# Kernel tuning notes

Hardware: AMD Instinct MI355X
Metric: run time of the kernel (lower is better)

The kernel has to match this reference:

```python
import jax, jax.numpy as jnp
import numpy as np

B, F, H, W = 1, 4, 20, 44
P = H * W            # 880 tokens per frame (20*44, from max_attention_size = 15*880)
S = F * P            # 3520 packed tokens
DIM, NH, FFN, OUT = 1536, 12, 6144, 64   # OUT = prod(patch_size)*out_dim = 4*16
HD = DIM // NH       # 128
C = HD // 2          # 64 rotary complex pairs
EPS = 1e-6


def _rope_angles():
    # Wan 3D RoPE: split C pairs as (C-2*(C//3), C//3, C//3) over (frame, h, w)
    cf, ch, cw = C - 2 * (C // 3), C // 3, C // 3
    def tab(n, cp):
        inv = 1.0 / (10000.0 ** (np.arange(cp) / cp))
        return np.outer(np.arange(n), inv)
    af = np.broadcast_to(tab(F, cf)[:, None, None, :], (F, H, W, cf))
    ah = np.broadcast_to(tab(H, ch)[None, :, None, :], (F, H, W, ch))
    aw = np.broadcast_to(tab(W, cw)[None, None, :, :], (F, H, W, cw))
    return np.concatenate([af, ah, aw], -1).reshape(S, C).astype(np.float32)


def setup_inputs() -> dict:
    key = jax.random.key(0)
    ks = jax.random.split(key, 24)
    g = lambda i, shape, s=0.02: jax.random.normal(ks[i], shape, dtype=jnp.float32) * s
    inp = {
        'x': jax.random.normal(ks[0], (B, S, DIM), dtype=jnp.float32),
        'e': g(1, (B, F, 6, DIM), 1.0),
        'e_head': g(2, (B, F, 2, DIM), 1.0),
        'rope_angles': jnp.asarray(_rope_angles()),
        'mod_block': g(3, (1, 6, DIM), 1.0 / float(np.sqrt(DIM))),
        'mod_head': g(4, (1, 2, DIM), 1.0 / float(np.sqrt(DIM))),
        'Wq': g(5, (DIM, DIM)), 'bq': jnp.zeros((DIM,), jnp.float32),
        'Wk': g(6, (DIM, DIM)), 'bk': jnp.zeros((DIM,), jnp.float32),
        'Wv': g(7, (DIM, DIM)), 'bv': jnp.zeros((DIM,), jnp.float32),
        'Wo': g(8, (DIM, DIM)), 'bo': jnp.zeros((DIM,), jnp.float32),
        'wq_norm': jnp.ones((DIM,), jnp.float32),
        'wk_norm': jnp.ones((DIM,), jnp.float32),
        'W1': g(9, (DIM, FFN)), 'b1': jnp.zeros((FFN,), jnp.float32),
        'W2': g(10, (FFN, DIM)), 'b2': jnp.zeros((DIM,), jnp.float32),
        'Wh': g(11, (DIM, OUT)), 'bh': jnp.zeros((OUT,), jnp.float32),
    }
    return inp


def _ln(x):
    # WanLayerNorm without elementwise affine
    m = jnp.mean(x, axis=-1, keepdims=True)
    v = jnp.var(x, axis=-1, keepdims=True)
    return (x - m) * jax.lax.rsqrt(v + EPS)


def _rms(x, w):
    return x * jax.lax.rsqrt(jnp.mean(x * x, axis=-1, keepdims=True) + EPS) * w


def _rope(t, ang):
    # t: [B,S,NH,HD]; adjacent pairs form complex numbers (view_as_complex style)
    tr = t.reshape(B, S, NH, C, 2)
    cos = jnp.cos(ang)[None, :, None, :]
    sin = jnp.sin(ang)[None, :, None, :]
    t0, t1 = tr[..., 0], tr[..., 1]
    return jnp.stack([t0 * cos - t1 * sin, t0 * sin + t1 * cos], -1).reshape(B, S, NH, HD)


def reference(x, e, e_head, rope_angles, mod_block, mod_head,
              Wq, bq, Wk, bk, Wv, bv, Wo, bo, wq_norm, wk_norm,
              W1, b1, W2, b2, Wh, bh):
    # ---- AdaLN modulation split (6-way) ----
    em = mod_block[:, None] + e                      # [B,F,6,DIM]
    e0, e1, e2, e3, e4, e5 = [em[:, :, i][:, :, None, :] for i in range(6)]

    xf = x.reshape(B, F, P, DIM)
    h = (_ln(xf) * (1 + e1) + e0).reshape(B, S, DIM)

    # ---- QK-RMSNorm + RoPE self attention (block-causal, block = one frame) ----
    q = _rope(_rms(h @ Wq + bq, wq_norm).reshape(B, S, NH, HD), rope_angles)
    k = _rope(_rms(h @ Wk + bk, wk_norm).reshape(B, S, NH, HD), rope_angles)
    v = (h @ Wv + bv).reshape(B, S, NH, HD)

    blk = jnp.arange(S) // P
    mask = blk[None, :] <= blk[:, None]              # [S,S] block-causal
    scores = jnp.einsum('bqhd,bkhd->bhqk', q, k) / np.float32(np.sqrt(HD))
    scores = jnp.where(mask[None, None], scores, jnp.float32(-1e30))
    attn = jax.nn.softmax(scores, axis=-1)
    y = jnp.einsum('bhqk,bkhd->bqhd', attn, v).reshape(B, S, DIM) @ Wo + bo

    xf = xf + y.reshape(B, F, P, DIM) * e2

    # ---- FFN with AdaLN modulation ----
    hf = (_ln(xf) * (1 + e4) + e3).reshape(B, S, DIM)
    ff = jax.nn.gelu(hf @ W1 + b1) @ W2 + b2
    xf = xf + ff.reshape(B, F, P, DIM) * e5

    # ---- OutputHead: modulated norm + linear ----
    eh = mod_head[:, None] + e_head                  # [B,F,2,DIM]
    eh0 = eh[:, :, 0][:, :, None, :]
    eh1 = eh[:, :, 1][:, :, None, :]
    out = (_ln(xf) * (1 + eh1) + eh0) @ Wh + bh      # [B,F,P,OUT]
    return out
```

## Files before the change

kernel.cpp:

```cpp
#include <hip/hip_runtime.h>
#include <cstdint>
#include <cstddef>

typedef __bf16 bf16;
typedef __bf16 bf16x2 __attribute__((ext_vector_type(2)));
typedef __bf16 bf16x8 __attribute__((ext_vector_type(8)));
typedef float f32x4 __attribute__((ext_vector_type(4)));
typedef unsigned int u32x4 __attribute__((ext_vector_type(4)));

#define S_TOK 3520
#define S_PAD 3584
#define P_TOK 880
#define NFRM 4
#define DIM 1536
#define NH 12
#define HD 128
#define FFN_D 6144
#define NOUT 64
#define EPSV 1e-6f
#define QSCALE 0.12751743f

__device__ __forceinline__ f32x4 mfma16(bf16x8 a, bf16x8 b, f32x4 c) {
  return __builtin_amdgcn_mfma_f32_16x16x32_bf16(a, b, c, 0, 0, 0);
}

__device__ __forceinline__ void gload_lds16(const bf16* g, bf16* l) {
  __builtin_amdgcn_global_load_lds(
      (const __attribute__((address_space(1))) unsigned int*)g,
      (__attribute__((address_space(3))) unsigned int*)l, 16, 0, 0);
}

__device__ __forceinline__ uint32_t pk2(float lo, float hi) {
  bf16x2 t;
  t[0] = (bf16)lo;
  t[1] = (bf16)hi;
  return __builtin_bit_cast(uint32_t, t);
}

__global__ __launch_bounds__(256) void k_prep(const float* __restrict__ e,
                                              const float* __restrict__ e_head,
                                              const float* __restrict__ mod_block,
                                              const float* __restrict__ mod_head,
                                              float* __restrict__ em,
                                              float* __restrict__ ehm) {
  int i = blockIdx.x * 256 + threadIdx.x;
  if (i < NFRM * 6 * DIM) em[i] = mod_block[i % (6 * DIM)] + e[i];
  int j = i - NFRM * 6 * DIM;
  if (j >= 0 && j < NFRM * 2 * DIM) ehm[j] = mod_head[j % (2 * DIM)] + e_head[j];
}

__global__ __launch_bounds__(256) void k_zero_vpad(bf16* __restrict__ vc) {
  size_t base = ((size_t)blockIdx.x * 28 + 27) * 4096 + 2048 + (size_t)threadIdx.x * 8;
#pragma unroll
  for (int i = 0; i < 8; ++i) vc[base + i] = (bf16)0.f;
}

__global__ __launch_bounds__(256) void k_transpose(const float* __restrict__ W,
                                                   bf16* __restrict__ Wt, int K, int N) {
  __shared__ float tile[32][33];
  int n0 = blockIdx.x * 32, k0 = blockIdx.y * 32;
  int tx = threadIdx.x & 31, ty = threadIdx.x >> 5;
#pragma unroll
  for (int j = 0; j < 4; ++j) {
    int k = k0 + ty * 4 + j;
    float v = (n0 + tx < N) ? W[(size_t)k * N + n0 + tx] : 0.f;
    tile[ty * 4 + j][tx] = v;
  }
  __syncthreads();
#pragma unroll
  for (int j = 0; j < 4; ++j) {
    int n = n0 + ty * 4 + j;
    if (n < N) Wt[(size_t)n * K + k0 + tx] = (bf16)tile[tx][ty * 4 + j];
  }
}

__global__ __launch_bounds__(256) void k_adaln(const float* __restrict__ in,
                                               bf16* __restrict__ out,
                                               const float* __restrict__ e_shift,
                                               const float* __restrict__ e_scale,
                                               int fstride) {
  int tok = blockIdx.x;
  int t = threadIdx.x;
  bf16* orow = out + (size_t)tok * DIM;
  if (tok >= S_TOK) {
#pragma unroll
    for (int i = 0; i < 6; ++i) orow[t * 6 + i] = (bf16)0.f;
    return;
  }
  const float* xrow = in + (size_t)tok * DIM;
  float v[6];
  float s = 0.f, sq = 0.f;
#pragma unroll
  for (int i = 0; i < 6; ++i) {
    v[i] = xrow[t * 6 + i];
    s += v[i];
    sq += v[i] * v[i];
  }
  for (int off = 32; off; off >>= 1) {
    s += __shfl_down(s, off);
    sq += __shfl_down(sq, off);
  }
  __shared__ float red[8];
  int wv = t >> 6, lane = t & 63;
  if (lane == 0) { red[wv] = s; red[4 + wv] = sq; }
  __syncthreads();
  float ts = red[0] + red[1] + red[2] + red[3];
  float tq = red[4] + red[5] + red[6] + red[7];
  float mean = ts * (1.f / DIM);
  float var = tq * (1.f / DIM) - mean * mean;
  float rstd = rsqrtf(var + EPSV);
  int f = tok / P_TOK;
  const float* sh = e_shift + (size_t)f * fstride;
  const float* sc = e_scale + (size_t)f * fstride;
#pragma unroll
  for (int i = 0; i < 6; ++i) {
    int d = t * 6 + i;
    orow[d] = (bf16)((v[i] - mean) * rstd * (1.f + sc[d]) + sh[d]);
  }
}

__global__ __launch_bounds__(256) void k_qkv_post(const float* __restrict__ qkv,
                                                  const float* __restrict__ wqn,
                                                  const float* __restrict__ wkn,
                                                  const float* __restrict__ ang,
                                                  bf16* __restrict__ qb,
                                                  bf16* __restrict__ kb,
                                                  bf16* __restrict__ vc) {
  int s = blockIdx.x;
  int t = threadIdx.x;
  const float* row = qkv + (size_t)s * 3 * DIM;
  float qv[6], kv[6], vv[6];
  float sqq = 0.f, sqk = 0.f;
  int d0 = t * 6;
#pragma unroll
  for (int i = 0; i < 6; ++i) {
    int d = d0 + i;
    qv[i] = row[d];
    kv[i] = row[DIM + d];
    vv[i] = row[2 * DIM + d];
    sqq += qv[i] * qv[i];
    sqk += kv[i] * kv[i];
  }
  float a1 = sqq, a2 = sqk;
  for (int off = 32; off; off >>= 1) {
    a1 += __shfl_down(a1, off);
    a2 += __shfl_down(a2, off);
  }
  __shared__ float red[8];
  int wv = t >> 6, lane = t & 63;
  if (lane == 0) { red[wv] = a1; red[4 + wv] = a2; }
  __syncthreads();
  float tq = red[0] + red[1] + red[2] + red[3];
  float tk = red[4] + red[5] + red[6] + red[7];
  float rq = rsqrtf(tq * (1.f / DIM) + EPSV);
  float rk = rsqrtf(tk * (1.f / DIM) + EPSV);
#pragma unroll
  for (int p = 0; p < 3; ++p) {
    int d = d0 + p * 2;
    int h = d >> 7;
    int hd = d & 127;
    int c = hd >> 1;
    float a = ang[(size_t)s * 64 + c];
    float sa, ca;
    sincosf(a, &sa, &ca);
    float q0 = qv[p * 2] * rq * wqn[d], q1 = qv[p * 2 + 1] * rq * wqn[d + 1];
    float k0 = kv[p * 2] * rk * wkn[d], k1 = kv[p * 2 + 1] * rk * wkn[d + 1];
    size_t base = ((size_t)h * S_TOK + s) * HD + hd;
    qb[base]     = (bf16)((q0 * ca - q1 * sa) * QSCALE);
    qb[base + 1] = (bf16)((q0 * sa + q1 * ca) * QSCALE);
    kb[base]     = (bf16)(k0 * ca - k1 * sa);
    kb[base + 1] = (bf16)(k0 * sa + k1 * ca);
  }
  int f = s / P_TOK;
  int l = s - f * P_TOK;
  int lb = l >> 5, gg = (l >> 3) & 3, r = l & 7;
#pragma unroll
  for (int i = 0; i < 6; ++i) {
    int d = d0 + i;
    int h = d >> 7, hd = d & 127;
    vc[((((size_t)(h * NFRM + f)) * 28 + lb) * 512 + gg * 128 + hd) * 8 + r] = (bf16)vv[i];
  }
}

__global__ __launch_bounds__(320) void k_attn(const bf16* __restrict__ qb,
                                              const bf16* __restrict__ kb,
                                              const bf16* __restrict__ vc,
                                              float* __restrict__ parto,
                                              float* __restrict__ partml) {
  __shared__ __align__(16) bf16 Ks[512 * 8];
  __shared__ __align__(16) bf16 Vs[512 * 8];
  int h = blockIdx.x / 110;
  int p = blockIdx.x % 110;
  int f = (p < 11) ? 0 : (p < 33) ? 1 : (p < 66) ? 2 : 3;
  int cum = (f == 0) ? 0 : (f == 1) ? 11 : (f == 2) ? 33 : 66;
  int w = p - cum;
  int kc = w / 11;
  int qt = f * 11 + w % 11;
  int slot = blockIdx.x;
  int t = threadIdx.x;
  int wv = t >> 6, lane = t & 63;
  int r16 = lane & 15, g = lane >> 4;
  int q0 = qt * 80 + wv * 16;
  int kv0 = kc * P_TOK;
  const bf16* qbase = qb + ((size_t)h * S_TOK + q0 + r16) * HD + g * 8;
  bf16x8 qf[4];
#pragma unroll
  for (int kk = 0; kk < 4; ++kk) qf[kk] = *(const bf16x8*)(qbase + kk * 32);
  f32x4 acc[8] = {};
  float mrow = -1e30f, lrow = 0.f;
  int src01 = r16 + ((2 * g) & 3) * 16;
  int src23 = src01 + 16;
  bool glo = (g < 2);
  int s1 = t + 320;
  bool has1 = (s1 < 512);
  int krow0 = t >> 4, ksl0 = t & 15;
  int kss0 = (ksl0 & 8) | ((ksl0 ^ krow0) & 7);
  int krow1 = s1 >> 4, ksl1 = s1 & 15;
  int kss1 = (ksl1 & 8) | ((ksl1 ^ krow1) & 7);
  const bf16* kh = kb + (size_t)h * S_TOK * HD;
  const bf16* vchunk = vc + ((size_t)(h * NFRM + kc)) * 28 * 4096;
  const int nsteps = (P_TOK + 31) >> 5;
  for (int j = 0; j < nsteps; ++j) {
    int kvo = j * 32;
    __syncthreads();
    {
      int gr0 = kv0 + kvo + krow0;
      if (gr0 >= S_TOK) gr0 = 0;
      gload_lds16(kh + (size_t)gr0 * HD + kss0 * 8, Ks + t * 8);
      gload_lds16(vchunk + (size_t)j * 4096 + t * 8, Vs + t * 8);
      if (has1) {
        int gr1 = kv0 + kvo + krow1;
        if (gr1 >= S_TOK) gr1 = 0;
        gload_lds16(kh + (size_t)gr1 * HD + kss1 * 8, Ks + s1 * 8);
        gload_lds16(vchunk + (size_t)j * 4096 + s1 * 8, Vs + s1 * 8);
      }
    }
    __syncthreads();
    f32x4 st0 = {0.f, 0.f, 0.f, 0.f}, st1 = {0.f, 0.f, 0.f, 0.f};
#pragma unroll
    for (int kk = 0; kk < 4; ++kk) {
      int sl = g + 4 * kk;
      int ss = (sl & 8) | ((sl ^ r16) & 7);
      bf16x8 k0 = *(const bf16x8*)(Ks + (r16 * 16 + ss) * 8);
      bf16x8 k1 = *(const bf16x8*)(Ks + ((16 + r16) * 16 + ss) * 8);
      st0 = mfma16(k0, qf[kk], st0);
      st1 = mfma16(k1, qf[kk], st1);
    }
    float hm = (kvo + 16 >= P_TOK) ? -1e30f : 0.f;
    float a0[4], a1[4];
#pragma unroll
    for (int r = 0; r < 4; ++r) {
      a0[r] = st0[r];
      a1[r] = st1[r] + hm;
    }
    float tm = fmaxf(fmaxf(fmaxf(a0[0], a0[1]), fmaxf(a0[2], a0[3])),
                     fmaxf(fmaxf(a1[0], a1[1]), fmaxf(a1[2], a1[3])));
    tm = fmaxf(tm, __shfl_xor(tm, 16));
    tm = fmaxf(tm, __shfl_xor(tm, 32));
    float mn = fmaxf(mrow, tm);
    float p0[4], p1[4], ps = 0.f;
#pragma unroll
    for (int r = 0; r < 4; ++r) {
      p0[r] = exp2f(a0[r] - mn);
      p1[r] = exp2f(a1[r] - mn);
      ps += p0[r] + p1[r];
    }
    float scl = exp2f(mrow - mn);
    mrow = mn;
    lrow = lrow * scl + ps;
    uint32_t A0 = pk2(p0[0], p0[1]), A1 = pk2(p0[2], p0[3]);
    uint32_t B0 = pk2(p1[0], p1[1]), B1 = pk2(p1[2], p1[3]);
    uint32_t sA0 = __shfl(A0, src01), sA1 = __shfl(A1, src01);
    uint32_t sB0 = __shfl(B0, src01), sB1 = __shfl(B1, src01);
    uint32_t tA0 = __shfl(A0, src23), tA1 = __shfl(A1, src23);
    uint32_t tB0 = __shfl(B0, src23), tB1 = __shfl(B1, src23);
    u32x4 wds;
    wds[0] = glo ? sA0 : sB0;
    wds[1] = glo ? sA1 : sB1;
    wds[2] = glo ? tA0 : tB0;
    wds[3] = glo ? tA1 : tB1;
    bf16x8 pb = __builtin_bit_cast(bf16x8, wds);
#pragma unroll
    for (int hb = 0; hb < 8; ++hb) {
      acc[hb][0] *= scl;
      acc[hb][1] *= scl;
      acc[hb][2] *= scl;
      acc[hb][3] *= scl;
    }
    const bf16* vsl = Vs + (size_t)(g * 128 + r16) * 8;
#pragma unroll
    for (int hb = 0; hb < 8; ++hb) {
      bf16x8 vfr = *(const bf16x8*)(vsl + hb * 128);
      acc[hb] = mfma16(vfr, pb, acc[hb]);
    }
  }
  lrow += __shfl_xor(lrow, 16);
  lrow += __shfl_xor(lrow, 32);
  float* obase = parto + (((size_t)slot * 5 + wv) * 8) * 256;
#pragma unroll
  for (int hb = 0; hb < 8; ++hb) {
    *(f32x4*)(obase + (hb * 64 + lane) * 4) = acc[hb];
  }
  if (g == 0) {
    float* mlb = partml + ((size_t)slot * 5 + wv) * 32;
    mlb[r16] = mrow;
    mlb[16 + r16] = lrow;
  }
}

__global__ __launch_bounds__(256) void k_att_reduce(const float* __restrict__ parto,
                                                    const float* __restrict__ partml,
                                                    bf16* __restrict__ attb) {
  int b = blockIdx.x;
  int h = b / 44, qt = b % 44;
  int f = qt / 11, j = qt % 11;
  int cum = (f == 0) ? 0 : (f == 1) ? 11 : (f == 2) ? 33 : 66;
  int t = threadIdx.x;
  int d = t & 127, half = t >> 7;
  int hb = d >> 4, g = (d >> 2) & 3, r = d & 3;
  int q0 = qt * 80;
  for (int it = 0; it < 40; ++it) {
    int qloc = it + 40 * half;
    int wv = qloc >> 4, r16 = qloc & 15;
    float m[4], l[4];
    float mt = -1e30f;
    for (int kc = 0; kc <= f; ++kc) {
      int slot = h * 110 + cum + kc * 11 + j;
      const float* mlb = partml + ((size_t)slot * 5 + wv) * 32;
      m[kc] = mlb[r16];
      l[kc] = mlb[16 + r16];
      mt = fmaxf(mt, m[kc]);
    }
    float lt = 0.f, o = 0.f;
    for (int kc = 0; kc <= f; ++kc) {
      int slot = h * 110 + cum + kc * 11 + j;
      float wgt = exp2f(m[kc] - mt);
      lt += l[kc] * wgt;
      o += parto[(((size_t)slot * 5 + wv) * 8 + hb) * 256 + (g * 16 + r16) * 4 + r] * wgt;
    }
    attb[(size_t)(q0 + qloc) * DIM + h * HD + d] = (bf16)(o / lt);
  }
}

struct GemmP {
  const bf16* A;
  const bf16* Bt;
  int K;
  int Mtiles;
  int Ntiles;
  int Mreal;
  int mode;
  const float* bias0;
  const float* bias1;
  const float* bias2;
  const float* res;
  const float* emod;
  int e_fstride;
  float* outf;
  bf16* outb;
  int ldo;
};

__global__ __launch_bounds__(256, 2) void k_gemm(GemmP p) {
  int nwg = p.Mtiles * p.Ntiles;
  int bid = blockIdx.x;
  int l = bid;
  if ((nwg & 7) == 0) {
    int cpx = nwg >> 3;
    l = (bid & 7) * cpx + (bid >> 3);
  }
  int bm = l % p.Mtiles;
  int bn = l / p.Mtiles;
  __shared__ __align__(16) bf16 As[2][128 * 32];
  __shared__ __align__(16) bf16 Bs[2][128 * 32];
  int t = threadIdx.x, lane = t & 63, wv = t >> 6;
  int r16 = lane & 15, g = lane >> 4;
  int wr = wv >> 1, wc = wv & 1;
  f32x4 acc[4][4] = {};
  const bf16* Ag = p.A + (size_t)bm * 128 * p.K;
  const bf16* Bg = p.Bt + (size_t)bn * 128 * p.K;
  int c0 = t, c1 = t + 256;
  int row0 = c0 >> 2, off0 = (c0 & 3) * 8;
  int row1 = c1 >> 2, off1 = (c1 & 3) * 8;
#define STAGE(buf, kk)                                                   \
  do {                                                                   \
    gload_lds16(Ag + (size_t)row0 * p.K + (kk) + off0, As[buf] + c0 * 8); \
    gload_lds16(Ag + (size_t)row1 * p.K + (kk) + off1, As[buf] + c1 * 8); \
    gload_lds16(Bg + (size_t)row0 * p.K + (kk) + off0, Bs[buf] + c0 * 8); \
    gload_lds16(Bg + (size_t)row1 * p.K + (kk) + off1, Bs[buf] + c1 * 8); \
  } while (0)
  const int nt = p.K >> 5;
  STAGE(0, 0);
  asm volatile("s_waitcnt vmcnt(0)" ::: "memory");
  __syncthreads();
  int cur = 0;
  for (int tt = 0; tt < nt; ++tt) {
    if (tt + 1 < nt) STAGE(cur ^ 1, (tt + 1) * 32);
    bf16x8 af[4], bfr[4];
#pragma unroll
    for (int mi = 0; mi < 4; ++mi)
      af[mi] = *(const bf16x8*)(As[cur] + (wr * 64 + mi * 16 + r16) * 32 + g * 8);
#pragma unroll
    for (int ni = 0; ni < 4; ++ni)
      bfr[ni] = *(const bf16x8*)(Bs[cur] + (wc * 64 + ni * 16 + r16) * 32 + g * 8);
#pragma unroll
    for (int mi = 0; mi < 4; ++mi)
#pragma unroll
      for (int ni = 0; ni < 4; ++ni)
        acc[mi][ni] = mfma16(af[mi], bfr[ni], acc[mi][ni]);
    asm volatile("s_waitcnt vmcnt(0)" ::: "memory");
    __syncthreads();
    cur ^= 1;
  }
#undef STAGE
  int mb = bm * 128 + wr * 64, nb0 = bn * 128 + wc * 64;
#pragma unroll
  for (int mi = 0; mi < 4; ++mi) {
#pragma unroll
    for (int ni = 0; ni < 4; ++ni) {
      int col = nb0 + ni * 16 + r16;
#pragma unroll
      for (int r = 0; r < 4; ++r) {
        int row = mb + mi * 16 + 4 * g + r;
        if (row >= p.Mreal) continue;
        float v = acc[mi][ni][r];
        if (p.mode == 0) {
          float b = col < DIM ? p.bias0[col]
                              : (col < 2 * DIM ? p.bias1[col - DIM] : p.bias2[col - 2 * DIM]);
          p.outf[(size_t)row * p.ldo + col] = v + b;
        } else if (p.mode == 1) {
          int fr = row / P_TOK;
          p.outf[(size_t)row * p.ldo + col] =
              p.res[(size_t)row * DIM + col] +
              (v + p.bias0[col]) * p.emod[(size_t)fr * p.e_fstride + col];
        } else if (p.mode == 2) {
          float xg = v + p.bias0[col];
          float gl = 0.5f * xg * (1.f + tanhf(0.7978845608028654f * (xg + 0.044715f * xg * xg * xg)));
          p.outb[(size_t)row * p.ldo + col] = (bf16)gl;
        } else {
          if (col < NOUT) p.outf[(size_t)row * p.ldo + col] = v + p.bias0[col];
        }
      }
    }
  }
}

extern "C" void kernel_launch(void* const* d_in, const int* in_sizes, int n_in,
                              void* d_out, int out_size, void* d_ws, size_t ws_size,
                              hipStream_t stream) {
  const float* x = (const float*)d_in[0];
  const float* e = (const float*)d_in[1];
  const float* e_head = (const float*)d_in[2];
  const float* ang = (const float*)d_in[3];
  const float* mod_block = (const float*)d_in[4];
  const float* mod_head = (const float*)d_in[5];
  const float* Wq = (const float*)d_in[6];
  const float* bq = (const float*)d_in[7];
  const float* Wk = (const float*)d_in[8];
  const float* bk = (const float*)d_in[9];
  const float* Wv = (const float*)d_in[10];
  const float* bv = (const float*)d_in[11];
  const float* Wo = (const float*)d_in[12];
  const float* bo = (const float*)d_in[13];
  const float* wqn = (const float*)d_in[14];
  const float* wkn = (const float*)d_in[15];
  const float* W1 = (const float*)d_in[16];
  const float* b1 = (const float*)d_in[17];
  const float* W2 = (const float*)d_in[18];
  const float* b2 = (const float*)d_in[19];
  const float* Wh = (const float*)d_in[20];
  const float* bh = (const float*)d_in[21];
  float* out = (float*)d_out;
  char* ws = (char*)d_ws;

  size_t WT_QKV = 0;
  size_t WT_O = WT_QKV + (size_t)3 * DIM * DIM * 2;
  size_t W1T = WT_O + (size_t)DIM * DIM * 2;
  size_t W2T = W1T + (size_t)FFN_D * DIM * 2;
  size_t WHT = W2T + (size_t)DIM * FFN_D * 2;
  size_t EMOFF = WHT + (size_t)128 * DIM * 2;
  size_t EHOFF = EMOFF + (size_t)NFRM * 6 * DIM * 4;
  size_t HB = EHOFF + (size_t)NFRM * 2 * DIM * 4;
  size_t CQKV = HB + (size_t)S_PAD * DIM * 2;
  size_t DQB = CQKV + (size_t)S_TOK * 3 * DIM * 4;
  size_t EATT = DQB + (size_t)3 * NH * S_TOK * HD * 2;
  size_t GXF2 = EATT + (size_t)S_PAD * DIM * 2;
  size_t END = GXF2 + (size_t)S_TOK * DIM * 4;
  if (ws_size < END) return;

  bf16* wtqkv = (bf16*)(ws + WT_QKV);
  bf16* wto = (bf16*)(ws + WT_O);
  bf16* w1t = (bf16*)(ws + W1T);
  bf16* w2t = (bf16*)(ws + W2T);
  bf16* wht = (bf16*)(ws + WHT);
  float* em = (float*)(ws + EMOFF);
  float* ehm = (float*)(ws + EHOFF);
  bf16* hb = (bf16*)(ws + HB);
  float* qkvf = (float*)(ws + CQKV);
  bf16* ffb = (bf16*)(ws + CQKV);
  float* parto = (float*)(ws + CQKV);
  float* partml = parto + (size_t)1320 * 5 * 8 * 256;
  bf16* qbp = (bf16*)(ws + DQB);
  bf16* kbp = qbp + (size_t)NH * S_TOK * HD;
  bf16* vcp = kbp + (size_t)NH * S_TOK * HD;
  float* xf3 = (float*)(ws + DQB);
  bf16* attb = (bf16*)(ws + EATT);
  float* xf2 = (float*)(ws + GXF2);

  k_prep<<<(NFRM * 8 * DIM) / 256, 256, 0, stream>>>(e, e_head, mod_block, mod_head, em, ehm);
  k_zero_vpad<<<NH * NFRM, 256, 0, stream>>>(vcp);

  k_transpose<<<dim3(48, 48), 256, 0, stream>>>(Wq, wtqkv, DIM, DIM);
  k_transpose<<<dim3(48, 48), 256, 0, stream>>>(Wk, wtqkv + (size_t)DIM * DIM, DIM, DIM);
  k_transpose<<<dim3(48, 48), 256, 0, stream>>>(Wv, wtqkv + (size_t)2 * DIM * DIM, DIM, DIM);
  k_transpose<<<dim3(48, 48), 256, 0, stream>>>(Wo, wto, DIM, DIM);
  k_transpose<<<dim3(192, 48), 256, 0, stream>>>(W1, w1t, DIM, FFN_D);
  k_transpose<<<dim3(48, 192), 256, 0, stream>>>(W2, w2t, FFN_D, DIM);
  k_transpose<<<dim3(2, 48), 256, 0, stream>>>(Wh, wht, DIM, NOUT);
  hipMemsetAsync(ws + WHT + (size_t)NOUT * DIM * 2, 0, (size_t)(128 - NOUT) * DIM * 2, stream);
  hipMemsetAsync(ws + EATT + (size_t)S_TOK * DIM * 2, 0, (size_t)(S_PAD - S_TOK) * DIM * 2, stream);

  k_adaln<<<S_PAD, 256, 0, stream>>>(x, hb, em, em + DIM, 6 * DIM);

  GemmP g0{};
  g0.A = hb; g0.Bt = wtqkv; g0.K = DIM; g0.Mtiles = 28; g0.Ntiles = 36; g0.Mreal = S_TOK;
  g0.mode = 0; g0.bias0 = bq; g0.bias1 = bk; g0.bias2 = bv; g0.outf = qkvf; g0.ldo = 3 * DIM;
  k_gemm<<<28 * 36, 256, 0, stream>>>(g0);

  k_qkv_post<<<S_TOK, 256, 0, stream>>>(qkvf, wqn, wkn, ang, qbp, kbp, vcp);

  k_attn<<<NH * 110, 320, 0, stream>>>(qbp, kbp, vcp, parto, partml);
  k_att_reduce<<<NH * 44, 256, 0, stream>>>(parto, partml, attb);

  GemmP g1{};
  g1.A = attb; g1.Bt = wto; g1.K = DIM; g1.Mtiles = 28; g1.Ntiles = 12; g1.Mreal = S_TOK;
  g1.mode = 1; g1.bias0 = bo; g1.res = x; g1.emod = em + 2 * DIM; g1.e_fstride = 6 * DIM;
  g1.outf = xf2; g1.ldo = DIM;
  k_gemm<<<28 * 12, 256, 0, stream>>>(g1);

  k_adaln<<<S_PAD, 256, 0, stream>>>(xf2, hb, em + 3 * DIM, em + 4 * DIM, 6 * DIM);

  GemmP g2{};
  g2.A = hb; g2.Bt = w1t; g2.K = DIM; g2.Mtiles = 28; g2.Ntiles = 48; g2.Mreal = S_TOK;
  g2.mode = 2; g2.bias0 = b1; g2.outb = ffb; g2.ldo = FFN_D;
  k_gemm<<<28 * 48, 256, 0, stream>>>(g2);
  hipMemsetAsync(ws + CQKV + (size_t)S_TOK * FFN_D * 2, 0, (size_t)(S_PAD - S_TOK) * FFN_D * 2, stream);

  GemmP g3{};
  g3.A = ffb; g3.Bt = w2t; g3.K = FFN_D; g3.Mtiles = 28; g3.Ntiles = 12; g3.Mreal = S_TOK;
  g3.mode = 1; g3.bias0 = b2; g3.res = xf2; g3.emod = em + 5 * DIM; g3.e_fstride = 6 * DIM;
  g3.outf = xf3; g3.ldo = DIM;
  k_gemm<<<28 * 12, 256, 0, stream>>>(g3);

  k_adaln<<<S_PAD, 256, 0, stream>>>(xf3, hb, ehm, ehm + DIM, 2 * DIM);

  GemmP g4{};
  g4.A = hb; g4.Bt = wht; g4.K = DIM; g4.Mtiles = 28; g4.Ntiles = 1; g4.Mreal = S_TOK;
  g4.mode = 4; g4.bias0 = bh; g4.outf = out; g4.ldo = NOUT;
  k_gemm<<<28, 256, 0, stream>>>(g4);
}
```

Baseline: 801.4 us.

## Double-buffer attention K/V staging and triple-buffer GEMM tiles with deeper prefetch

The attention kernel now double-buffers its K and V LDS tiles. It prefetches the next 32-key chunk with the first 256 threads while the current chunk is computed, and replaces the two full __syncthreads per step with vmcnt waits plus raw barriers. The GEMM kernel moves from a double to a triple LDS buffer with two tiles in flight, uses partial vmcnt waits, and raises the launch bound minimum to 3 blocks. The aim is to hide global-to-LDS load latency behind MFMA work. In exchange, LDS per block grows and register budgets tighten, which risks spills or lower occupancy.

```diff
diff --git a/kernel.cpp b/kernel.cpp
--- a/kernel.cpp
+++ b/kernel.cpp
@@ -187,8 +187,8 @@
                                               const bf16* __restrict__ vc,
                                               float* __restrict__ parto,
                                               float* __restrict__ partml) {
-  __shared__ __align__(16) bf16 Ks[512 * 8];
-  __shared__ __align__(16) bf16 Vs[512 * 8];
+  __shared__ __align__(16) bf16 Ks[2][512 * 8];
+  __shared__ __align__(16) bf16 Vs[2][512 * 8];
   int h = blockIdx.x / 110;
   int p = blockIdx.x % 110;
   int f = (p < 11) ? 0 : (p < 33) ? 1 : (p < 66) ? 2 : 3;
@@ -211,38 +211,42 @@
   int src01 = r16 + ((2 * g) & 3) * 16;
   int src23 = src01 + 16;
   bool glo = (g < 2);
-  int s1 = t + 320;
-  bool has1 = (s1 < 512);
-  int krow0 = t >> 4, ksl0 = t & 15;
-  int kss0 = (ksl0 & 8) | ((ksl0 ^ krow0) & 7);
-  int krow1 = s1 >> 4, ksl1 = s1 & 15;
-  int kss1 = (ksl1 & 8) | ((ksl1 ^ krow1) & 7);
+  int sB = t + 256;
+  int kr0 = t >> 4, kl0 = t & 15;
+  int ks0 = (kl0 & 8) | ((kl0 ^ kr0) & 7);
+  int kr1 = sB >> 4, kl1 = sB & 15;
+  int ks1 = (kl1 & 8) | ((kl1 ^ kr1) & 7);
   const bf16* kh = kb + (size_t)h * S_TOK * HD;
   const bf16* vchunk = vc + ((size_t)(h * NFRM + kc)) * 28 * 4096;
+#define STAGE_ATT(buf, jj)                                                  \
+  do {                                                                      \
+    int kvoj = (jj) * 32;                                                   \
+    int gr0 = kv0 + kvoj + kr0; if (gr0 >= S_TOK) gr0 = 0;                  \
+    int gr1 = kv0 + kvoj + kr1; if (gr1 >= S_TOK) gr1 = 0;                  \
+    gload_lds16(kh + (size_t)gr0 * HD + ks0 * 8, Ks[buf] + t * 8);          \
+    gload_lds16(kh + (size_t)gr1 * HD + ks1 * 8, Ks[buf] + sB * 8);         \
+    gload_lds16(vchunk + (size_t)(jj) * 4096 + t * 8, Vs[buf] + t * 8);     \
+    gload_lds16(vchunk + (size_t)(jj) * 4096 + sB * 8, Vs[buf] + sB * 8);   \
+  } while (0)
   const int nsteps = (P_TOK + 31) >> 5;
+  if (t < 256) STAGE_ATT(0, 0);
+  int cur = 0;
   for (int j = 0; j < nsteps; ++j) {
     int kvo = j * 32;
-    __syncthreads();
-    {
-      int gr0 = kv0 + kvo + krow0;
-      if (gr0 >= S_TOK) gr0 = 0;
-      gload_lds16(kh + (size_t)gr0 * HD + kss0 * 8, Ks + t * 8);
-      gload_lds16(vchunk + (size_t)j * 4096 + t * 8, Vs + t * 8);
-      if (has1) {
-        int gr1 = kv0 + kvo + krow1;
-        if (gr1 >= S_TOK) gr1 = 0;
-        gload_lds16(kh + (size_t)gr1 * HD + kss1 * 8, Ks + s1 * 8);
-        gload_lds16(vchunk + (size_t)j * 4096 + s1 * 8, Vs + s1 * 8);
-      }
-    }
-    __syncthreads();
+    if (j + 1 < nsteps) {
+      if (t < 256) STAGE_ATT(cur ^ 1, j + 1);
+      asm volatile("s_waitcnt vmcnt(4)" ::: "memory");
+    } else {
+      asm volatile("s_waitcnt vmcnt(0)" ::: "memory");
+    }
+    __builtin_amdgcn_s_barrier();
     f32x4 st0 = {0.f, 0.f, 0.f, 0.f}, st1 = {0.f, 0.f, 0.f, 0.f};
 #pragma unroll
     for (int kk = 0; kk < 4; ++kk) {
       int sl = g + 4 * kk;
       int ss = (sl & 8) | ((sl ^ r16) & 7);
-      bf16x8 k0 = *(const bf16x8*)(Ks + (r16 * 16 + ss) * 8);
-      bf16x8 k1 = *(const bf16x8*)(Ks + ((16 + r16) * 16 + ss) * 8);
+      bf16x8 k0 = *(const bf16x8*)(Ks[cur] + (r16 * 16 + ss) * 8);
+      bf16x8 k1 = *(const bf16x8*)(Ks[cur] + ((16 + r16) * 16 + ss) * 8);
       st0 = mfma16(k0, qf[kk], st0);
       st1 = mfma16(k1, qf[kk], st1);
     }
@@ -287,13 +291,17 @@
       acc[hb][2] *= scl;
       acc[hb][3] *= scl;
     }
-    const bf16* vsl = Vs + (size_t)(g * 128 + r16) * 8;
+    const bf16* vsl = Vs[cur] + (size_t)(g * 128 + r16) * 8;
 #pragma unroll
     for (int hb = 0; hb < 8; ++hb) {
       bf16x8 vfr = *(const bf16x8*)(vsl + hb * 128);
       acc[hb] = mfma16(vfr, pb, acc[hb]);
     }
-  }
+    asm volatile("" ::: "memory");
+    __builtin_amdgcn_s_barrier();
+    cur ^= 1;
+  }
+#undef STAGE_ATT
   lrow += __shfl_xor(lrow, 16);
   lrow += __shfl_xor(lrow, 32);
   float* obase = parto + (((size_t)slot * 5 + wv) * 8) * 256;
@@ -361,7 +369,7 @@
   int ldo;
 };
 
-__global__ __launch_bounds__(256, 2) void k_gemm(GemmP p) {
+__global__ __launch_bounds__(256, 3) void k_gemm(GemmP p) {
   int nwg = p.Mtiles * p.Ntiles;
   int bid = blockIdx.x;
   int l = bid;
@@ -371,8 +379,8 @@
   }
   int bm = l % p.Mtiles;
   int bn = l / p.Mtiles;
-  __shared__ __align__(16) bf16 As[2][128 * 32];
-  __shared__ __align__(16) bf16 Bs[2][128 * 32];
+  __shared__ __align__(16) bf16 As[3][128 * 32];
+  __shared__ __align__(16) bf16 Bs[3][128 * 32];
   int t = threadIdx.x, lane = t & 63, wv = t >> 6;
   int r16 = lane & 15, g = lane >> 4;
   int wr = wv >> 1, wc = wv & 1;
@@ -382,20 +390,30 @@
   int c0 = t, c1 = t + 256;
   int row0 = c0 >> 2, off0 = (c0 & 3) * 8;
   int row1 = c1 >> 2, off1 = (c1 & 3) * 8;
-#define STAGE(buf, kk)                                                   \
-  do {                                                                   \
-    gload_lds16(Ag + (size_t)row0 * p.K + (kk) + off0, As[buf] + c0 * 8); \
-    gload_lds16(Ag + (size_t)row1 * p.K + (kk) + off1, As[buf] + c1 * 8); \
-    gload_lds16(Bg + (size_t)row0 * p.K + (kk) + off0, Bs[buf] + c0 * 8); \
-    gload_lds16(Bg + (size_t)row1 * p.K + (kk) + off1, Bs[buf] + c1 * 8); \
+#define STAGE(buf, kk)                                                     \
+  do {                                                                     \
+    gload_lds16(Ag + (size_t)row0 * p.K + (kk) + off0, As[buf] + c0 * 8);  \
+    gload_lds16(Ag + (size_t)row1 * p.K + (kk) + off1, As[buf] + c1 * 8);  \
+    gload_lds16(Bg + (size_t)row0 * p.K + (kk) + off0, Bs[buf] + c0 * 8);  \
+    gload_lds16(Bg + (size_t)row1 * p.K + (kk) + off1, Bs[buf] + c1 * 8);  \
   } while (0)
   const int nt = p.K >> 5;
   STAGE(0, 0);
-  asm volatile("s_waitcnt vmcnt(0)" ::: "memory");
-  __syncthreads();
+  STAGE(1, 32);
   int cur = 0;
   for (int tt = 0; tt < nt; ++tt) {
-    if (tt + 1 < nt) STAGE(cur ^ 1, (tt + 1) * 32);
+    int rem = nt - 1 - tt;
+    if (rem >= 2) {
+      int nb = cur + 2;
+      if (nb >= 3) nb -= 3;
+      STAGE(nb, (tt + 2) * 32);
+      asm volatile("s_waitcnt vmcnt(8)" ::: "memory");
+    } else if (rem == 1) {
+      asm volatile("s_waitcnt vmcnt(4)" ::: "memory");
+    } else {
+      asm volatile("s_waitcnt vmcnt(0)" ::: "memory");
+    }
+    __builtin_amdgcn_s_barrier();
     bf16x8 af[4], bfr[4];
 #pragma unroll
     for (int mi = 0; mi < 4; ++mi)
@@ -408,9 +426,9 @@
 #pragma unroll
       for (int ni = 0; ni < 4; ++ni)
         acc[mi][ni] = mfma16(af[mi], bfr[ni], acc[mi][ni]);
-    asm volatile("s_waitcnt vmcnt(0)" ::: "memory");
-    __syncthreads();
-    cur ^= 1;
+    asm volatile("" ::: "memory");
+    __builtin_amdgcn_s_barrier();
+    cur = (cur + 1 == 3) ? 0 : cur + 1;
   }
 #undef STAGE
   int mb = bm * 128 + wr * 64, nb0 = bn * 128 + wc * 64;
```

Result: no change. 803.0 us (+0.2%).
